# Performance work log

Hardware: AMD Instinct MI355X
Metric: run time of the kernel (lower is better)

Reference implementation:

```python
import jax, jax.numpy as jnp
import numpy as np

NUM_USER = 100000
NUM_ENT = 200000
NUM_REL = 32
DIM = 64
N_NEIGHBOR = 16
BATCH = 16384


def setup_inputs() -> dict:
    key = jax.random.key(0)
    ks = jax.random.split(key, 11)
    inp = {
        "u": jax.random.randint(ks[0], (BATCH,), 0, NUM_USER),
        "v": jax.random.randint(ks[1], (BATCH,), 0, NUM_ENT),
        "user_neighbor": jax.random.randint(ks[2], (BATCH, N_NEIGHBOR), 0, NUM_ENT),
        "item_neighbor": jax.random.randint(ks[3], (BATCH, N_NEIGHBOR), 0, NUM_USER),
        "adj_ent": jax.random.randint(ks[4], (NUM_ENT, N_NEIGHBOR), 0, NUM_ENT),
        "adj_rel": jax.random.randint(ks[5], (NUM_ENT, N_NEIGHBOR), 0, NUM_REL),
        "usr_emb": jax.random.normal(ks[6], (NUM_USER, DIM), dtype=jnp.float32) * 0.1,
        "ent_emb": jax.random.normal(ks[7], (NUM_ENT, DIM), dtype=jnp.float32) * 0.1,
        "rel_emb": jax.random.normal(ks[8], (NUM_REL, DIM), dtype=jnp.float32) * 0.1,
        "agg_W": jax.random.normal(ks[9], (DIM, DIM), dtype=jnp.float32) * (1.0 / np.sqrt(DIM)),
        "agg_b": jax.random.normal(ks[10], (DIM,), dtype=jnp.float32) * 0.01,
    }
    return inp


def reference(u, v, user_neighbor, item_neighbor, adj_ent, adj_rel,
              usr_emb, ent_emb, rel_emb, agg_W, agg_b):
    n = N_NEIGHBOR
    # LightGCN-style "lite" embeddings: mean over sampled interaction neighbors
    lite_user = usr_emb[item_neighbor].sum(axis=1) * (1.0 / n)   # [B, D]
    lite_item = ent_emb[user_neighbor].sum(axis=1) * (1.0 / n)   # [B, D]

    user_embeddings = usr_emb[u]                                  # [B, D]
    item_embeddings_original = ent_emb[v]                         # [B, D]

    # one-hop KG neighbors of items
    nbr_ent = adj_ent[v]                                          # [B, n]
    nbr_rel = adj_rel[v]                                          # [B, n]
    self_vectors = item_embeddings_original[:, None, :]           # [B, 1, D]
    neighbor_vectors = ent_emb[nbr_ent][:, None, :, :]            # [B, 1, n, D]
    neighbor_relations = rel_emb[nbr_rel][:, None, :, :]          # [B, 1, n, D]

    # KGCN sum-aggregator: user-relation attention over neighbors
    ur_scores = jnp.einsum("bd,bknd->bkn", user_embeddings, neighbor_relations)
    attn = jax.nn.softmax(ur_scores, axis=-1)                     # [B, 1, n]
    neighbors_agg = jnp.einsum("bkn,bknd->bkd", attn, neighbor_vectors)
    combined = self_vectors + neighbors_agg                       # [B, 1, D]
    item_embeddings = jnp.tanh(combined @ agg_W + agg_b)[:, 0, :]  # [B, D]

    user_final = 0.5 * lite_user + 0.5 * user_embeddings
    item_final = 0.5 * lite_item + 0.5 * item_embeddings
    scores = jnp.sum(user_final * item_final, axis=1)
    return jax.nn.sigmoid(scores)
```

## Files before the change

kernel.cpp:

```cpp
#include <hip/hip_runtime.h>
#include <math.h>

#define DIM 64
#define NNB 16
#define BATCH 16384

typedef float4 f4;

__device__ __forceinline__ float dot4(const f4 a, const f4 b) {
    return fmaf(a.x, b.x, fmaf(a.y, b.y, fmaf(a.z, b.z, a.w * b.w)));
}

__device__ __forceinline__ f4 xgrp_sum(f4 v) {
    v.x += __shfl_xor(v.x, 16, 64); v.y += __shfl_xor(v.y, 16, 64);
    v.z += __shfl_xor(v.z, 16, 64); v.w += __shfl_xor(v.w, 16, 64);
    v.x += __shfl_xor(v.x, 32, 64); v.y += __shfl_xor(v.y, 32, 64);
    v.z += __shfl_xor(v.z, 32, 64); v.w += __shfl_xor(v.w, 32, 64);
    return v;
}

template <int WPB>
__global__ __launch_bounds__(WPB * 64, 3) void klgcn_kernel(
    const int* __restrict__ u, const int* __restrict__ v,
    const int* __restrict__ user_neighbor, const int* __restrict__ item_neighbor,
    const int* __restrict__ adj_ent, const int* __restrict__ adj_rel,
    const float* __restrict__ usr_emb, const float* __restrict__ ent_emb,
    const float* __restrict__ rel_emb, const float* __restrict__ agg_W,
    const float* __restrict__ agg_b, float* __restrict__ out)
{
    const int wave = threadIdx.x >> 6;
    const int lane = threadIdx.x & 63;
    const int g = lane >> 4;
    const int s = lane & 15;
    const int b0 = __builtin_amdgcn_readfirstlane((blockIdx.x * WPB + wave) * 2);
    const int bb[2] = {b0, b0 + 1};

    const f4* __restrict__ usr4 = (const f4*)usr_emb;
    const f4* __restrict__ ent4 = (const f4*)ent_emb;
    const f4* __restrict__ rel4 = (const f4*)rel_emb;
    const f4* __restrict__ W4   = (const f4*)agg_W;
    const f4* __restrict__ b4p  = (const f4*)agg_b;
    const int4* __restrict__ it4 = (const int4*)item_neighbor;
    const int4* __restrict__ un4 = (const int4*)user_neighbor;
    const int4* __restrict__ ar4 = (const int4*)adj_rel;
    const int4* __restrict__ ae4 = (const int4*)adj_ent;

    int ub[2], vb[2];
#pragma unroll
    for (int el = 0; el < 2; el++) {
        ub[el] = __builtin_amdgcn_readfirstlane(u[bb[el]]);
        vb[el] = __builtin_amdgcn_readfirstlane(v[bb[el]]);
    }

    int4 iit[2], iun[2], iar[2], iae[2];
#pragma unroll
    for (int el = 0; el < 2; el++) {
        iit[el] = it4[bb[el] * 4 + g];
        iun[el] = un4[bb[el] * 4 + g];
        iar[el] = ar4[vb[el] * 4 + g];
        iae[el] = ae4[vb[el] * 4 + g];
    }

    f4 ue4[2], ie4[2];
#pragma unroll
    for (int el = 0; el < 2; el++) {
        ue4[el] = usr4[(long)ub[el] * 16 + s];
        ie4[el] = ent4[(long)vb[el] * 16 + s];
    }

    f4 Re[2][4], Ag[2][4], Lu[2][4], Li[2][4];
#pragma unroll
    for (int el = 0; el < 2; el++) {
        Re[el][0] = rel4[iar[el].x * 16 + s];
        Re[el][1] = rel4[iar[el].y * 16 + s];
        Re[el][2] = rel4[iar[el].z * 16 + s];
        Re[el][3] = rel4[iar[el].w * 16 + s];
    }
#pragma unroll
    for (int el = 0; el < 2; el++) {
        Ag[el][0] = ent4[(long)iae[el].x * 16 + s];
        Ag[el][1] = ent4[(long)iae[el].y * 16 + s];
        Ag[el][2] = ent4[(long)iae[el].z * 16 + s];
        Ag[el][3] = ent4[(long)iae[el].w * 16 + s];
    }
#pragma unroll
    for (int el = 0; el < 2; el++) {
        Lu[el][0] = usr4[(long)iit[el].x * 16 + s];
        Lu[el][1] = usr4[(long)iit[el].y * 16 + s];
        Lu[el][2] = usr4[(long)iit[el].z * 16 + s];
        Lu[el][3] = usr4[(long)iit[el].w * 16 + s];
    }
#pragma unroll
    for (int el = 0; el < 2; el++) {
        Li[el][0] = ent4[(long)iun[el].x * 16 + s];
        Li[el][1] = ent4[(long)iun[el].y * 16 + s];
        Li[el][2] = ent4[(long)iun[el].z * 16 + s];
        Li[el][3] = ent4[(long)iun[el].w * 16 + s];
    }

    float e[2][4], inv[2];
#pragma unroll
    for (int el = 0; el < 2; el++) {
        float sc[4];
#pragma unroll
        for (int k = 0; k < 4; k++) {
            float p = dot4(ue4[el], Re[el][k]);
            p += __shfl_xor(p, 1, 64); p += __shfl_xor(p, 2, 64);
            p += __shfl_xor(p, 4, 64); p += __shfl_xor(p, 8, 64);
            sc[k] = p;
        }
        float m = fmaxf(fmaxf(sc[0], sc[1]), fmaxf(sc[2], sc[3]));
        m = fmaxf(m, __shfl_xor(m, 16, 64));
        m = fmaxf(m, __shfl_xor(m, 32, 64));
        float ssum = 0.f;
#pragma unroll
        for (int k = 0; k < 4; k++) { e[el][k] = __expf(sc[k] - m); ssum += e[el][k]; }
        ssum += __shfl_xor(ssum, 16, 64);
        ssum += __shfl_xor(ssum, 32, 64);
        inv[el] = 1.0f / ssum;
    }

    float cc[2][4];
#pragma unroll
    for (int el = 0; el < 2; el++) {
        f4 ag = {0.f, 0.f, 0.f, 0.f};
#pragma unroll
        for (int k = 0; k < 4; k++) {
            ag.x = fmaf(e[el][k], Ag[el][k].x, ag.x);
            ag.y = fmaf(e[el][k], Ag[el][k].y, ag.y);
            ag.z = fmaf(e[el][k], Ag[el][k].z, ag.z);
            ag.w = fmaf(e[el][k], Ag[el][k].w, ag.w);
        }
        ag = xgrp_sum(ag);
        cc[el][0] = fmaf(ag.x, inv[el], ie4[el].x);
        cc[el][1] = fmaf(ag.y, inv[el], ie4[el].y);
        cc[el][2] = fmaf(ag.z, inv[el], ie4[el].z);
        cc[el][3] = fmaf(ag.w, inv[el], ie4[el].w);
    }

    f4 lu[2], li[2];
#pragma unroll
    for (int el = 0; el < 2; el++) {
        f4 t;
        t.x = Lu[el][0].x + Lu[el][1].x + Lu[el][2].x + Lu[el][3].x;
        t.y = Lu[el][0].y + Lu[el][1].y + Lu[el][2].y + Lu[el][3].y;
        t.z = Lu[el][0].z + Lu[el][1].z + Lu[el][2].z + Lu[el][3].z;
        t.w = Lu[el][0].w + Lu[el][1].w + Lu[el][2].w + Lu[el][3].w;
        lu[el] = xgrp_sum(t);
        t.x = Li[el][0].x + Li[el][1].x + Li[el][2].x + Li[el][3].x;
        t.y = Li[el][0].y + Li[el][1].y + Li[el][2].y + Li[el][3].y;
        t.z = Li[el][0].z + Li[el][1].z + Li[el][2].z + Li[el][3].z;
        t.w = Li[el][0].w + Li[el][1].w + Li[el][2].w + Li[el][3].w;
        li[el] = xgrp_sum(t);
    }

    f4 acc[2] = {{0.f, 0.f, 0.f, 0.f}, {0.f, 0.f, 0.f, 0.f}};
#pragma unroll
    for (int j = 0; j < 16; j++) {
        const int d = 16 * g + j;
        const f4 w = W4[d * 16 + s];
        const int src = 20 * g + (j >> 2);
#pragma unroll
        for (int el = 0; el < 2; el++) {
            const float cd = __shfl(cc[el][j & 3], src, 64);
            acc[el].x = fmaf(cd, w.x, acc[el].x);
            acc[el].y = fmaf(cd, w.y, acc[el].y);
            acc[el].z = fmaf(cd, w.z, acc[el].z);
            acc[el].w = fmaf(cd, w.w, acc[el].w);
        }
    }
    const f4 bias = b4p[s];
    float res[2];
#pragma unroll
    for (int el = 0; el < 2; el++) {
        acc[el] = xgrp_sum(acc[el]);
        f4 item4;
        item4.x = tanhf(acc[el].x + bias.x);
        item4.y = tanhf(acc[el].y + bias.y);
        item4.z = tanhf(acc[el].z + bias.z);
        item4.w = tanhf(acc[el].w + bias.w);

        f4 uf, itf;
        uf.x = 0.5f * fmaf(lu[el].x, 1.f / NNB, ue4[el].x);
        uf.y = 0.5f * fmaf(lu[el].y, 1.f / NNB, ue4[el].y);
        uf.z = 0.5f * fmaf(lu[el].z, 1.f / NNB, ue4[el].z);
        uf.w = 0.5f * fmaf(lu[el].w, 1.f / NNB, ue4[el].w);
        itf.x = 0.5f * fmaf(li[el].x, 1.f / NNB, item4.x);
        itf.y = 0.5f * fmaf(li[el].y, 1.f / NNB, item4.y);
        itf.z = 0.5f * fmaf(li[el].z, 1.f / NNB, item4.z);
        itf.w = 0.5f * fmaf(li[el].w, 1.f / NNB, item4.w);

        float p = dot4(uf, itf);
        p += __shfl_xor(p, 1, 64); p += __shfl_xor(p, 2, 64);
        p += __shfl_xor(p, 4, 64); p += __shfl_xor(p, 8, 64);
        res[el] = 1.0f / (1.0f + __expf(-p));
    }

    if (lane == 0) {
        *(float2*)(out + b0) = make_float2(res[0], res[1]);
    }
}

extern "C" void kernel_launch(void* const* d_in, const int* in_sizes, int n_in,
                              void* d_out, int out_size, void* d_ws, size_t ws_size,
                              hipStream_t stream)
{
    const int*   u             = (const int*)d_in[0];
    const int*   v             = (const int*)d_in[1];
    const int*   user_neighbor = (const int*)d_in[2];
    const int*   item_neighbor = (const int*)d_in[3];
    const int*   adj_ent       = (const int*)d_in[4];
    const int*   adj_rel       = (const int*)d_in[5];
    const float* usr_emb       = (const float*)d_in[6];
    const float* ent_emb       = (const float*)d_in[7];
    const float* rel_emb       = (const float*)d_in[8];
    const float* agg_W         = (const float*)d_in[9];
    const float* agg_b         = (const float*)d_in[10];
    float* out = (float*)d_out;

    constexpr int WPB = 4;
    dim3 grid(BATCH / (WPB * 2)), block(WPB * 64);
    klgcn_kernel<WPB><<<grid, block, 0, stream>>>(
        u, v, user_neighbor, item_neighbor, adj_ent, adj_rel,
        usr_emb, ent_emb, rel_emb, agg_W, agg_b, out);
}
```

Baseline: 151.9 us.

## Stage agg_W and rel_emb in LDS with swizzled layout

Each block now cooperatively copies the full 64x64 aggregator weight matrix and the 32-row relation table into shared memory, then reads W and relation vectors from LDS instead of global/L2. W uses an XOR swizzle and rel rows are padded to limit bank conflicts. The launch-bounds occupancy hint rises from 3 to 4 blocks per CU. In exchange every block pays about 26KB of LDS, a cooperative load and a barrier before the gathers, which may limit occupancy and delays the issue of the latency-bound embedding gathers.

```diff
diff --git a/kernel.cpp b/kernel.cpp
--- a/kernel.cpp
+++ b/kernel.cpp
@@ -19,8 +19,12 @@
     return v;
 }
 
+__device__ __forceinline__ int wslot(int d, int sIdx) {
+    return d * 16 + (sIdx ^ ((d >> 2) & 15));
+}
+
 template <int WPB>
-__global__ __launch_bounds__(WPB * 64, 3) void klgcn_kernel(
+__global__ __launch_bounds__(WPB * 64, 4) void klgcn_kernel(
     const int* __restrict__ u, const int* __restrict__ v,
     const int* __restrict__ user_neighbor, const int* __restrict__ item_neighbor,
     const int* __restrict__ adj_ent, const int* __restrict__ adj_rel,
@@ -28,8 +32,12 @@
     const float* __restrict__ rel_emb, const float* __restrict__ agg_W,
     const float* __restrict__ agg_b, float* __restrict__ out)
 {
-    const int wave = threadIdx.x >> 6;
-    const int lane = threadIdx.x & 63;
+    __shared__ f4 ldsW[1024];
+    __shared__ f4 ldsRel[32 * 17];
+
+    const int t = threadIdx.x;
+    const int wave = t >> 6;
+    const int lane = t & 63;
     const int g = lane >> 4;
     const int s = lane & 15;
     const int b0 = __builtin_amdgcn_readfirstlane((blockIdx.x * WPB + wave) * 2);
@@ -68,14 +76,19 @@
         ie4[el] = ent4[(long)vb[el] * 16 + s];
     }
 
-    f4 Re[2][4], Ag[2][4], Lu[2][4], Li[2][4];
-#pragma unroll
-    for (int el = 0; el < 2; el++) {
-        Re[el][0] = rel4[iar[el].x * 16 + s];
-        Re[el][1] = rel4[iar[el].y * 16 + s];
-        Re[el][2] = rel4[iar[el].z * 16 + s];
-        Re[el][3] = rel4[iar[el].w * 16 + s];
-    }
+#pragma unroll
+    for (int k = 0; k < 4; k++) {
+        const int c = t + 256 * k;
+        ldsW[wslot(c >> 4, c & 15)] = W4[c];
+    }
+#pragma unroll
+    for (int k = 0; k < 2; k++) {
+        const int c = t + 256 * k;
+        ldsRel[(c >> 4) * 17 + (c & 15)] = rel4[c];
+    }
+    __syncthreads();
+
+    f4 Ag[2][4], Lu[2][4], Li[2][4];
 #pragma unroll
     for (int el = 0; el < 2; el++) {
         Ag[el][0] = ent4[(long)iae[el].x * 16 + s];
@@ -101,10 +114,12 @@
     float e[2][4], inv[2];
 #pragma unroll
     for (int el = 0; el < 2; el++) {
+        const int rid[4] = {iar[el].x, iar[el].y, iar[el].z, iar[el].w};
         float sc[4];
 #pragma unroll
         for (int k = 0; k < 4; k++) {
-            float p = dot4(ue4[el], Re[el][k]);
+            const f4 re = ldsRel[rid[k] * 17 + s];
+            float p = dot4(ue4[el], re);
             p += __shfl_xor(p, 1, 64); p += __shfl_xor(p, 2, 64);
             p += __shfl_xor(p, 4, 64); p += __shfl_xor(p, 8, 64);
             sc[k] = p;
@@ -141,24 +156,24 @@
     f4 lu[2], li[2];
 #pragma unroll
     for (int el = 0; el < 2; el++) {
-        f4 t;
-        t.x = Lu[el][0].x + Lu[el][1].x + Lu[el][2].x + Lu[el][3].x;
-        t.y = Lu[el][0].y + Lu[el][1].y + Lu[el][2].y + Lu[el][3].y;
-        t.z = Lu[el][0].z + Lu[el][1].z + Lu[el][2].z + Lu[el][3].z;
-        t.w = Lu[el][0].w + Lu[el][1].w + Lu[el][2].w + Lu[el][3].w;
-        lu[el] = xgrp_sum(t);
-        t.x = Li[el][0].x + Li[el][1].x + Li[el][2].x + Li[el][3].x;
-        t.y = Li[el][0].y + Li[el][1].y + Li[el][2].y + Li[el][3].y;
-        t.z = Li[el][0].z + Li[el][1].z + Li[el][2].z + Li[el][3].z;
-        t.w = Li[el][0].w + Li[el][1].w + Li[el][2].w + Li[el][3].w;
-        li[el] = xgrp_sum(t);
+        f4 tt;
+        tt.x = Lu[el][0].x + Lu[el][1].x + Lu[el][2].x + Lu[el][3].x;
+        tt.y = Lu[el][0].y + Lu[el][1].y + Lu[el][2].y + Lu[el][3].y;
+        tt.z = Lu[el][0].z + Lu[el][1].z + Lu[el][2].z + Lu[el][3].z;
+        tt.w = Lu[el][0].w + Lu[el][1].w + Lu[el][2].w + Lu[el][3].w;
+        lu[el] = xgrp_sum(tt);
+        tt.x = Li[el][0].x + Li[el][1].x + Li[el][2].x + Li[el][3].x;
+        tt.y = Li[el][0].y + Li[el][1].y + Li[el][2].y + Li[el][3].y;
+        tt.z = Li[el][0].z + Li[el][1].z + Li[el][2].z + Li[el][3].z;
+        tt.w = Li[el][0].w + Li[el][1].w + Li[el][2].w + Li[el][3].w;
+        li[el] = xgrp_sum(tt);
     }
 
     f4 acc[2] = {{0.f, 0.f, 0.f, 0.f}, {0.f, 0.f, 0.f, 0.f}};
 #pragma unroll
     for (int j = 0; j < 16; j++) {
         const int d = 16 * g + j;
-        const f4 w = W4[d * 16 + s];
+        const f4 w = ldsW[wslot(d, s)];
         const int src = 20 * g + (j >> 2);
 #pragma unroll
         for (int el = 0; el < 2; el++) {
```

Measured after the change: 165.8 us. 9.1% more time.
